# Kernel tuning notes

Measured on AMD Instinct MI355X. Metric: run time of the kernel, lower is better.

The kernel has to match this reference:

```python
import jax, jax.numpy as jnp
import numpy as np

B, S, D = 2, 2048, 1024
H, HD = 16, 64  # num_heads, hidden_size per head


def setup_inputs() -> dict:
    key = jax.random.key(0)
    ks = jax.random.split(key, 10)
    inp = {
        'queries': jax.random.normal(ks[0], (B, S, D), jnp.float32),
        'keys': jax.random.normal(ks[1], (B, S, D), jnp.float32),
        'values': jax.random.normal(ks[2], (B, S, D), jnp.float32),
        # binary indicator masks (some zeros so renorm guard path is exercised)
        'ind_q': (jax.random.uniform(ks[3], (B, S)) > 0.2).astype(jnp.float32),
        'ind_k': (jax.random.uniform(ks[4], (B, S)) > 0.2).astype(jnp.float32),
        'ind_v': (jax.random.uniform(ks[5], (B, S)) > 0.2).astype(jnp.float32),
        'Wq': jax.random.normal(ks[6], (D, H * HD), jnp.float32) / np.sqrt(D),
        'Wk': jax.random.normal(ks[7], (D, H * HD), jnp.float32) / np.sqrt(D),
        'Wv': jax.random.normal(ks[8], (D, H * HD), jnp.float32) / np.sqrt(D),
        'Wo': jax.random.normal(ks[9], (H * HD, D), jnp.float32) / np.sqrt(H * HD),
    }
    return inp


def reference(queries, keys, values, ind_q, ind_k, ind_v, Wq, Wk, Wv, Wo):
    b, nq, _ = queries.shape
    nk = keys.shape[1]
    # projections -> [B, H, S, HD], masked by indicators
    Q = (queries @ Wq).reshape(b, nq, H, HD).transpose(0, 2, 1, 3) * ind_q[:, None, :, None]
    K = (keys @ Wk).reshape(b, nk, H, HD).transpose(0, 2, 1, 3) * ind_k[:, None, :, None]
    V = (values @ Wv).reshape(b, nk, H, HD).transpose(0, 2, 1, 3) * ind_v[:, None, :, None]
    # scaled dot-product scores, plain softmax over keys
    scores = jnp.einsum('bhqd,bhkd->bhqk', Q, K) / jnp.sqrt(jnp.float32(HD))
    attn = jax.nn.softmax(scores, axis=-1)
    # post-softmax multiplicative key-indicator mask + renormalization with zero-row guard
    attn = attn * ind_k[:, None, None, :]
    denom = jnp.sum(attn, axis=-1, keepdims=True)
    attn = attn / jnp.where(denom == 0.0, 1.0, denom)
    out = jnp.einsum('bhqk,bhkd->bhqd', attn, V)  # [B, H, Q, HD]
    out = out.transpose(0, 2, 1, 3).reshape(b, nq, H * HD)
    return out @ Wo
```

## Files before the change

### kernel.cpp

```cpp
#include <hip/hip_runtime.h>
#include <math.h>

typedef __attribute__((ext_vector_type(8))) short bf16x8;
typedef __attribute__((ext_vector_type(4))) float f32x4;

__device__ __forceinline__ unsigned short f2b(float f) {
    union { float f; unsigned int u; } v; v.f = f;
    unsigned int u = v.u + 0x7FFFu + ((v.u >> 16) & 1u);
    return (unsigned short)(u >> 16);
}

__device__ __forceinline__ f32x4 mfma16(bf16x8 a, bf16x8 b, f32x4 c) {
    return __builtin_amdgcn_mfma_f32_16x16x32_bf16(a, b, c, 0, 0, 0);
}

__device__ __forceinline__ void async_ld16(void* l, const void* g) {
    __builtin_amdgcn_global_load_lds(
        (__attribute__((address_space(1))) void*)g,
        (__attribute__((address_space(3))) void*)l, 16, 0, 0);
}

__device__ __forceinline__ float exp2_hw(float x) {
    float r; asm("v_exp_f32 %0, %1" : "=v"(r) : "v"(x)); return r;
}

__device__ __forceinline__ unsigned int cvtpk_bf16(float a, float b) {
    unsigned int r;
    asm("v_cvt_pk_bf16_f32 %0, %1, %2" : "=v"(r) : "v"(a), "v"(b));
    return r;
}

__global__ __launch_bounds__(256) void cvt3(
    const float* __restrict__ q, const float* __restrict__ k,
    const float* __restrict__ v, unsigned short* __restrict__ qo,
    unsigned short* __restrict__ ko, unsigned short* __restrict__ vo)
{
    const int z = blockIdx.z;
    const float* in = (z == 0) ? q : (z == 1) ? k : v;
    unsigned short* out = (z == 0) ? qo : (z == 1) ? ko : vo;
    const int i = (blockIdx.x * 256 + threadIdx.x) * 4;
    const float4 x = *(const float4*)(in + i);
    ushort4 o; o.x = f2b(x.x); o.y = f2b(x.y); o.z = f2b(x.z); o.w = f2b(x.w);
    *(ushort4*)(out + i) = o;
}

__global__ __launch_bounds__(256) void cvt_tr(
    const float* __restrict__ W0, const float* __restrict__ W1,
    const float* __restrict__ W2, const float* __restrict__ W3,
    unsigned short* __restrict__ T0, unsigned short* __restrict__ T1,
    unsigned short* __restrict__ T2, unsigned short* __restrict__ T3)
{
    const int z = blockIdx.z;
    const float* W = (z == 0) ? W0 : (z == 1) ? W1 : (z == 2) ? W2 : W3;
    unsigned short* T = (z == 0) ? T0 : (z == 1) ? T1 : (z == 2) ? T2 : T3;
    __shared__ short Ls[64 * 65];
    const int t = threadIdx.x;
    const int k0 = blockIdx.x * 64, n0 = blockIdx.y * 64;
#pragma unroll
    for (int ii = 0; ii < 4; ++ii) {
        const int kl = (t >> 4) + 16 * ii, nl = (t & 15) * 4;
        const float4 v = *(const float4*)&W[(size_t)(k0 + kl) * 1024 + n0 + nl];
        Ls[kl * 65 + nl + 0] = (short)f2b(v.x);
        Ls[kl * 65 + nl + 1] = (short)f2b(v.y);
        Ls[kl * 65 + nl + 2] = (short)f2b(v.z);
        Ls[kl * 65 + nl + 3] = (short)f2b(v.w);
    }
    __syncthreads();
#pragma unroll
    for (int ii = 0; ii < 4; ++ii) {
        const int nl = (t >> 4) + 16 * ii, kl = (t & 15) * 4;
        ushort4 o;
        o.x = (unsigned short)Ls[(kl + 0) * 65 + nl];
        o.y = (unsigned short)Ls[(kl + 1) * 65 + nl];
        o.z = (unsigned short)Ls[(kl + 2) * 65 + nl];
        o.w = (unsigned short)Ls[(kl + 3) * 65 + nl];
        *(ushort4*)&T[(size_t)(n0 + nl) * 1024 + k0 + kl] = o;
    }
}

__global__ __launch_bounds__(256) void gemm_proj3(
    const unsigned short* __restrict__ qb, const unsigned short* __restrict__ kb,
    const unsigned short* __restrict__ vb,
    const unsigned short* __restrict__ Wqt, const unsigned short* __restrict__ Wkt,
    const unsigned short* __restrict__ Wvt,
    unsigned short* __restrict__ Qw, unsigned short* __restrict__ Kw,
    unsigned short* __restrict__ Vw,
    const float* __restrict__ iq, const float* __restrict__ ik,
    const float* __restrict__ iv)
{
    const int z = blockIdx.z;
    const unsigned short* A  = (z == 0) ? qb  : (z == 1) ? kb  : vb;
    const unsigned short* Bt = (z == 0) ? Wqt : (z == 1) ? Wkt : Wvt;
    unsigned short* Cw       = (z == 0) ? Qw  : (z == 1) ? Kw  : Vw;
    const float* msk         = (z == 0) ? iq  : (z == 1) ? ik  : iv;
    const float scale = (z == 0) ? 0.125f * 1.44269504088896f : 1.0f;

    __shared__ __align__(16) short As[128 * 32];
    __shared__ __align__(16) short Bs[128 * 32];
    __shared__ float maskL[128];
    const int t = threadIdx.x;
    const int w = t >> 6, lane = t & 63, l15 = lane & 15, quad = lane >> 4;
    const int wr = w >> 1, wc = w & 1;
    const int n0 = blockIdx.x * 128, m0 = blockIdx.y * 128;
    if (t < 128) maskL[t] = msk[m0 + t] * scale;

    const int srow = lane >> 2, soff = (lane & 3) * 8;

    f32x4 zero4 = {0.f, 0.f, 0.f, 0.f};
    f32x4 acc[4][4];
#pragma unroll
    for (int i = 0; i < 4; ++i)
#pragma unroll
        for (int j = 0; j < 4; ++j) acc[i][j] = zero4;

    for (int k0 = 0; k0 < 1024; k0 += 32) {
        __syncthreads();
#pragma unroll
        for (int i = 0; i < 2; ++i) {
            const int r = 16 * (2 * w + i);
            async_ld16(As + r * 32, A + (size_t)(m0 + r + srow) * 1024 + k0 + soff);
            async_ld16(Bs + r * 32, Bt + (size_t)(n0 + r + srow) * 1024 + k0 + soff);
        }
        __syncthreads();
        bf16x8 af[4], bfr[4];
#pragma unroll
        for (int i = 0; i < 4; ++i)
            af[i] = *(const bf16x8*)&As[(64 * wr + 16 * i + l15) * 32 + 8 * quad];
#pragma unroll
        for (int j = 0; j < 4; ++j)
            bfr[j] = *(const bf16x8*)&Bs[(64 * wc + 16 * j + l15) * 32 + 8 * quad];
#pragma unroll
        for (int i = 0; i < 4; ++i)
#pragma unroll
            for (int j = 0; j < 4; ++j)
                acc[i][j] = mfma16(af[i], bfr[j], acc[i][j]);
    }

    const int h = 2 * blockIdx.x + wc;
#pragma unroll
    for (int i = 0; i < 4; ++i)
#pragma unroll
        for (int j = 0; j < 4; ++j)
#pragma unroll
            for (int reg = 0; reg < 4; ++reg) {
                const int mloc = 64 * wr + 16 * i + 4 * quad + reg;
                const int m = m0 + mloc;
                const int bb = m >> 11, s = m & 2047;
                const int hd = 16 * j + l15;
                Cw[((size_t)(bb * 16 + h) * 2048 + s) * 64 + hd] =
                    f2b(acc[i][j][reg] * maskL[mloc]);
            }
}

__global__ __launch_bounds__(256) void gemm_out(
    const unsigned short* __restrict__ A, const unsigned short* __restrict__ Bt,
    float* __restrict__ C)
{
    __shared__ __align__(16) short As[128 * 32];
    __shared__ __align__(16) short Bs[64 * 32];
    const int t = threadIdx.x;
    const int w = t >> 6, lane = t & 63, l15 = lane & 15, quad = lane >> 4;
    const int wr = w >> 1, wc = w & 1;
    const int n0 = blockIdx.x * 64, m0 = blockIdx.y * 128;
    const int srow = lane >> 2, soff = (lane & 3) * 8;

    f32x4 zero4 = {0.f, 0.f, 0.f, 0.f};
    f32x4 acc[4][2];
#pragma unroll
    for (int i = 0; i < 4; ++i) { acc[i][0] = zero4; acc[i][1] = zero4; }

    for (int k0 = 0; k0 < 1024; k0 += 32) {
        __syncthreads();
#pragma unroll
        for (int i = 0; i < 2; ++i) {
            const int r = 16 * (2 * w + i);
            async_ld16(As + r * 32, A + (size_t)(m0 + r + srow) * 1024 + k0 + soff);
        }
        async_ld16(Bs + (16 * w) * 32, Bt + (size_t)(n0 + 16 * w + srow) * 1024 + k0 + soff);
        __syncthreads();
        bf16x8 af[4], bfr[2];
#pragma unroll
        for (int i = 0; i < 4; ++i)
            af[i] = *(const bf16x8*)&As[(64 * wr + 16 * i + l15) * 32 + 8 * quad];
#pragma unroll
        for (int j = 0; j < 2; ++j)
            bfr[j] = *(const bf16x8*)&Bs[(32 * wc + 16 * j + l15) * 32 + 8 * quad];
#pragma unroll
        for (int i = 0; i < 4; ++i)
#pragma unroll
            for (int j = 0; j < 2; ++j)
                acc[i][j] = mfma16(af[i], bfr[j], acc[i][j]);
    }
#pragma unroll
    for (int i = 0; i < 4; ++i)
#pragma unroll
        for (int j = 0; j < 2; ++j)
#pragma unroll
            for (int reg = 0; reg < 4; ++reg) {
                const int m = m0 + 64 * wr + 16 * i + 4 * quad + reg;
                const int n = n0 + 32 * wc + 16 * j + l15;
                C[(size_t)m * 1024 + n] = acc[i][j][reg];
            }
}

#define GST 72

__global__ __launch_bounds__(512, 4) void attn_mfma(
    const unsigned short* __restrict__ Qw, const unsigned short* __restrict__ Kw,
    const unsigned short* __restrict__ Vw, const float* __restrict__ indk,
    unsigned short* __restrict__ AO)
{
    __shared__ __align__(16) short Ks[2][64 * GST];
    __shared__ __align__(16) short Vt[2][64 * GST];
    __shared__ float Bl[2048];
    const int t = threadIdx.x;
    const int w = t >> 6, lane = t & 63, l15 = lane & 15, quad = lane >> 4;
    const unsigned wg = (blockIdx.x & 7) * 64 + (blockIdx.x >> 3);
    const int q0 = (wg & 15) * 128;
    const int h = (wg >> 4) & 15, b = wg >> 8;
    const size_t base = (size_t)(b * 16 + h) * (2048 * 64);
    const unsigned short* Qb = Qw + base + (size_t)q0 * 64;
    const unsigned short* Kb = Kw + base;
    const unsigned short* Vb = Vw + base;

    bf16x8 qf[2];
    qf[0] = *(const bf16x8*)&Qb[(16 * w + l15) * 64 + 8 * quad];
    qf[1] = *(const bf16x8*)&Qb[(16 * w + l15) * 64 + 32 + 8 * quad];

    {
        const float4 bi = *(const float4*)&indk[b * 2048 + t * 4];
        float4 bo;
        bo.x = (bi.x - 1.f) * 1e30f; bo.y = (bi.y - 1.f) * 1e30f;
        bo.z = (bi.z - 1.f) * 1e30f; bo.w = (bi.w - 1.f) * 1e30f;
        *(float4*)&Bl[t * 4] = bo;
    }

    const int skr = t >> 3, skc = (t & 7) * 8;
    const int slr = skr ^ (((skr >> 3) & 1) << 2);
    const int dq = t >> 5, kp2 = (t & 31) * 2;

    bf16x8 kreg;
    ushort4 vreg[2];
    kreg = *(const bf16x8*)&Kb[(size_t)skr * 64 + skc];
    vreg[0] = *(const ushort4*)&Vb[(size_t)kp2 * 64 + 4 * dq];
    vreg[1] = *(const ushort4*)&Vb[(size_t)(kp2 + 1) * 64 + 4 * dq];

    const int u_ = l15 >> 2, a_ = l15 & 3;
    const int krA = 8 * u_ + 4 * (u_ & 1) + a_;
    const int krB = 8 * u_ + 4 * (1 - (u_ & 1)) + a_;

    f32x4 zero4 = {0.f, 0.f, 0.f, 0.f};
    f32x4 oacc[4];
    oacc[0] = zero4; oacc[1] = zero4; oacc[2] = zero4; oacc[3] = zero4;
    float l_part = 0.f;

    for (int c = 0; c < 32; ++c) {
        const int cur = c & 1;
        *(bf16x8*)&Ks[cur][slr * GST + skc] = kreg;
        {
            const unsigned int* v0d = (const unsigned int*)&vreg[0];
            const unsigned int* v1d = (const unsigned int*)&vreg[1];
            *(unsigned int*)&Vt[cur][(4 * dq + 0) * GST + kp2] =
                __builtin_amdgcn_perm(v1d[0], v0d[0], 0x05040100u);
            *(unsigned int*)&Vt[cur][(4 * dq + 1) * GST + kp2] =
                __builtin_amdgcn_perm(v1d[0], v0d[0], 0x07060302u);
            *(unsigned int*)&Vt[cur][(4 * dq + 2) * GST + kp2] =
                __builtin_amdgcn_perm(v1d[1], v0d[1], 0x05040100u);
            *(unsigned int*)&Vt[cur][(4 * dq + 3) * GST + kp2] =
                __builtin_amdgcn_perm(v1d[1], v0d[1], 0x07060302u);
        }
        __syncthreads();
        {
            const int kn = (c < 31 ? c + 1 : 31) * 64;
            kreg = *(const bf16x8*)&Kb[(size_t)(kn + skr) * 64 + skc];
            vreg[0] = *(const ushort4*)&Vb[(size_t)(kn + kp2) * 64 + 4 * dq];
            vreg[1] = *(const ushort4*)&Vb[(size_t)(kn + kp2 + 1) * 64 + 4 * dq];
        }
        const short* KsC = Ks[cur];
        const short* VtC = Vt[cur];
        const float* BlC = Bl + c * 64;

        f32x4 sacc[4];
#pragma unroll
        for (int g = 0; g < 4; ++g) {
            const float4 bv = *(const float4*)&BlC[32 * (g >> 1) + 4 * (g & 1) + 8 * quad];
            sacc[g][0] = bv.x; sacc[g][1] = bv.y; sacc[g][2] = bv.z; sacc[g][3] = bv.w;
        }
        __builtin_amdgcn_s_setprio(1);
#pragma unroll
        for (int ks = 0; ks < 2; ++ks)
#pragma unroll
            for (int g = 0; g < 4; ++g) {
                const int row = 32 * (g >> 1) + ((g & 1) ? krB : krA);
                const bf16x8 kf = *(const bf16x8*)&KsC[row * GST + 32 * ks + 8 * quad];
                sacc[g] = mfma16(kf, qf[ks], sacc[g]);
            }
        __builtin_amdgcn_s_setprio(0);

        unsigned int dw[4][2];
#pragma unroll
        for (int g = 0; g < 4; ++g) {
#pragma unroll
            for (int r = 0; r < 4; ++r) sacc[g][r] = exp2_hw(sacc[g][r]);
            dw[g][0] = cvtpk_bf16(sacc[g][0], sacc[g][1]);
            dw[g][1] = cvtpk_bf16(sacc[g][2], sacc[g][3]);
        }

        __builtin_amdgcn_s_setprio(1);
#pragma unroll
        for (int ks = 0; ks < 2; ++ks) {
            union { unsigned int u[4]; bf16x8 b; } pc;
            pc.u[0] = dw[2 * ks][0];     pc.u[1] = dw[2 * ks][1];
            pc.u[2] = dw[2 * ks + 1][0]; pc.u[3] = dw[2 * ks + 1][1];
#pragma unroll
            for (int nj = 0; nj < 4; ++nj) {
                const bf16x8 vbf = *(const bf16x8*)
                    &VtC[(16 * nj + l15) * GST + 32 * ks + 8 * quad];
                oacc[nj] = mfma16(pc.b, vbf, oacc[nj]);
            }
        }
        __builtin_amdgcn_s_setprio(0);

        float rg[4];
#pragma unroll
        for (int g = 0; g < 4; ++g)
            rg[g] = (sacc[g][0] + sacc[g][1]) + (sacc[g][2] + sacc[g][3]);
        l_part += (rg[0] + rg[1]) + (rg[2] + rg[3]);
    }

    float l = l_part;
    l += __shfl_xor(l, 16);
    l += __shfl_xor(l, 32);
    const float inv = (l > 0.f) ? 1.f / l : 0.f;
    float invr[4];
#pragma unroll
    for (int r = 0; r < 4; ++r) invr[r] = __shfl(inv, 4 * quad + r);
#pragma unroll
    for (int nj = 0; nj < 4; ++nj)
#pragma unroll
        for (int r = 0; r < 4; ++r) {
            const int row = q0 + 16 * w + 4 * quad + r;
            AO[(size_t)(b * 2048 + row) * 1024 + h * 64 + 16 * nj + l15] =
                f2b(oacc[nj][r] * invr[r]);
        }
}

extern "C" void kernel_launch(void* const* d_in, const int* in_sizes, int n_in,
                              void* d_out, int out_size, void* d_ws, size_t ws_size,
                              hipStream_t stream) {
    const float* q  = (const float*)d_in[0];
    const float* k  = (const float*)d_in[1];
    const float* v  = (const float*)d_in[2];
    const float* iq = (const float*)d_in[3];
    const float* ik = (const float*)d_in[4];
    const float* iv = (const float*)d_in[5];
    const float* Wq = (const float*)d_in[6];
    const float* Wk = (const float*)d_in[7];
    const float* Wv = (const float*)d_in[8];
    const float* Wo = (const float*)d_in[9];
    float* out = (float*)d_out;
    unsigned short* ws = (unsigned short*)d_ws;

    const size_t M1 = 1048576;
    unsigned short* qb  = ws;
    unsigned short* kb  = ws + 4  * M1;
    unsigned short* vb  = ws + 8  * M1;
    unsigned short* Wqt = ws + 12 * M1;
    unsigned short* Wkt = ws + 13 * M1;
    unsigned short* Wvt = ws + 14 * M1;
    unsigned short* Wot = ws + 15 * M1;
    unsigned short* Qw  = ws + 16 * M1;
    unsigned short* Kw  = ws + 20 * M1;
    unsigned short* Vw  = ws + 24 * M1;
    unsigned short* AO  = ws + 28 * M1;

    cvt3<<<dim3(4096, 1, 3), dim3(256), 0, stream>>>(q, k, v, qb, kb, vb);
    cvt_tr<<<dim3(16, 16, 4), dim3(256), 0, stream>>>(Wq, Wk, Wv, Wo, Wqt, Wkt, Wvt, Wot);
    gemm_proj3<<<dim3(8, 32, 3), dim3(256), 0, stream>>>(
        qb, kb, vb, Wqt, Wkt, Wvt, Qw, Kw, Vw, iq, ik, iv);
    attn_mfma<<<dim3(512, 1, 1), dim3(512), 0, stream>>>(Qw, Kw, Vw, ik, AO);
    gemm_out<<<dim3(16, 32), dim3(256), 0, stream>>>(AO, Wot, out);
}
```

Before: 227.4 us.

## Fuse fp32-to-bf16 input conversion into projection GEMM with register-prefetched double buffering

Drops the separate cvt3 kernel and has the projection GEMM read fp32 activations directly, converting them to bf16 in registers before storing to LDS. The main loop now uses double-buffered LDS, with register prefetch of the next K-slice replacing async global-to-LDS loads, and raises wave priority around the MFMA block. This removes one kernel launch plus the write and re-read of a bf16 copy of q/k/v. In exchange, the GEMM reads twice as many bytes for A, uses more registers and LDS, and does the conversion work redundantly across the 8 column blocks.

```diff
diff --git a/kernel.cpp b/kernel.cpp
--- a/kernel.cpp
+++ b/kernel.cpp
@@ -28,20 +28,6 @@
     unsigned int r;
     asm("v_cvt_pk_bf16_f32 %0, %1, %2" : "=v"(r) : "v"(a), "v"(b));
     return r;
-}
-
-__global__ __launch_bounds__(256) void cvt3(
-    const float* __restrict__ q, const float* __restrict__ k,
-    const float* __restrict__ v, unsigned short* __restrict__ qo,
-    unsigned short* __restrict__ ko, unsigned short* __restrict__ vo)
-{
-    const int z = blockIdx.z;
-    const float* in = (z == 0) ? q : (z == 1) ? k : v;
-    unsigned short* out = (z == 0) ? qo : (z == 1) ? ko : vo;
-    const int i = (blockIdx.x * 256 + threadIdx.x) * 4;
-    const float4 x = *(const float4*)(in + i);
-    ushort4 o; o.x = f2b(x.x); o.y = f2b(x.y); o.z = f2b(x.z); o.w = f2b(x.w);
-    *(ushort4*)(out + i) = o;
 }
 
 __global__ __launch_bounds__(256) void cvt_tr(
@@ -79,8 +65,8 @@
 }
 
 __global__ __launch_bounds__(256) void gemm_proj3(
-    const unsigned short* __restrict__ qb, const unsigned short* __restrict__ kb,
-    const unsigned short* __restrict__ vb,
+    const float* __restrict__ qf, const float* __restrict__ kf,
+    const float* __restrict__ vf,
     const unsigned short* __restrict__ Wqt, const unsigned short* __restrict__ Wkt,
     const unsigned short* __restrict__ Wvt,
     unsigned short* __restrict__ Qw, unsigned short* __restrict__ Kw,
@@ -89,14 +75,14 @@
     const float* __restrict__ iv)
 {
     const int z = blockIdx.z;
-    const unsigned short* A  = (z == 0) ? qb  : (z == 1) ? kb  : vb;
+    const float* A           = (z == 0) ? qf  : (z == 1) ? kf  : vf;
     const unsigned short* Bt = (z == 0) ? Wqt : (z == 1) ? Wkt : Wvt;
     unsigned short* Cw       = (z == 0) ? Qw  : (z == 1) ? Kw  : Vw;
     const float* msk         = (z == 0) ? iq  : (z == 1) ? ik  : iv;
     const float scale = (z == 0) ? 0.125f * 1.44269504088896f : 1.0f;
 
-    __shared__ __align__(16) short As[128 * 32];
-    __shared__ __align__(16) short Bs[128 * 32];
+    __shared__ __align__(16) short As[2][128 * 32];
+    __shared__ __align__(16) short Bs[2][128 * 32];
     __shared__ float maskL[128];
     const int t = threadIdx.x;
     const int w = t >> 6, lane = t & 63, l15 = lane & 15, quad = lane >> 4;
@@ -104,7 +90,18 @@
     const int n0 = blockIdx.x * 128, m0 = blockIdx.y * 128;
     if (t < 128) maskL[t] = msk[m0 + t] * scale;
 
-    const int srow = lane >> 2, soff = (lane & 3) * 8;
+    const int ar = t >> 1, ac = (t & 1) * 16;
+    const float* Arow          = A  + (size_t)(m0 + ar) * 1024 + ac;
+    const unsigned short* Brow = Bt + (size_t)(n0 + ar) * 1024 + ac;
+
+    float4 a4[4];
+    bf16x8 b8[2];
+    a4[0] = *(const float4*)(Arow + 0);
+    a4[1] = *(const float4*)(Arow + 4);
+    a4[2] = *(const float4*)(Arow + 8);
+    a4[3] = *(const float4*)(Arow + 12);
+    b8[0] = *(const bf16x8*)(Brow + 0);
+    b8[1] = *(const bf16x8*)(Brow + 8);
 
     f32x4 zero4 = {0.f, 0.f, 0.f, 0.f};
     f32x4 acc[4][4];
@@ -113,27 +110,43 @@
 #pragma unroll
         for (int j = 0; j < 4; ++j) acc[i][j] = zero4;
 
-    for (int k0 = 0; k0 < 1024; k0 += 32) {
+    for (int step = 0; step < 32; ++step) {
+        const int cur = step & 1;
+        {
+            uint4 lo, hi;
+            lo.x = cvtpk_bf16(a4[0].x, a4[0].y); lo.y = cvtpk_bf16(a4[0].z, a4[0].w);
+            lo.z = cvtpk_bf16(a4[1].x, a4[1].y); lo.w = cvtpk_bf16(a4[1].z, a4[1].w);
+            hi.x = cvtpk_bf16(a4[2].x, a4[2].y); hi.y = cvtpk_bf16(a4[2].z, a4[2].w);
+            hi.z = cvtpk_bf16(a4[3].x, a4[3].y); hi.w = cvtpk_bf16(a4[3].z, a4[3].w);
+            *(uint4*)&As[cur][ar * 32 + ac]     = lo;
+            *(uint4*)&As[cur][ar * 32 + ac + 8] = hi;
+            *(bf16x8*)&Bs[cur][ar * 32 + ac]     = b8[0];
+            *(bf16x8*)&Bs[cur][ar * 32 + ac + 8] = b8[1];
+        }
         __syncthreads();
-#pragma unroll
-        for (int i = 0; i < 2; ++i) {
-            const int r = 16 * (2 * w + i);
-            async_ld16(As + r * 32, A + (size_t)(m0 + r + srow) * 1024 + k0 + soff);
-            async_ld16(Bs + r * 32, Bt + (size_t)(n0 + r + srow) * 1024 + k0 + soff);
-        }
-        __syncthreads();
+        {
+            const int kn = (step < 31 ? step + 1 : 31) * 32;
+            a4[0] = *(const float4*)(Arow + kn + 0);
+            a4[1] = *(const float4*)(Arow + kn + 4);
+            a4[2] = *(const float4*)(Arow + kn + 8);
+            a4[3] = *(const float4*)(Arow + kn + 12);
+            b8[0] = *(const bf16x8*)(Brow + kn + 0);
+            b8[1] = *(const bf16x8*)(Brow + kn + 8);
+        }
         bf16x8 af[4], bfr[4];
 #pragma unroll
         for (int i = 0; i < 4; ++i)
-            af[i] = *(const bf16x8*)&As[(64 * wr + 16 * i + l15) * 32 + 8 * quad];
+            af[i] = *(const bf16x8*)&As[cur][(64 * wr + 16 * i + l15) * 32 + 8 * quad];
 #pragma unroll
         for (int j = 0; j < 4; ++j)
-            bfr[j] = *(const bf16x8*)&Bs[(64 * wc + 16 * j + l15) * 32 + 8 * quad];
+            bfr[j] = *(const bf16x8*)&Bs[cur][(64 * wc + 16 * j + l15) * 32 + 8 * quad];
+        __builtin_amdgcn_s_setprio(1);
 #pragma unroll
         for (int i = 0; i < 4; ++i)
 #pragma unroll
             for (int j = 0; j < 4; ++j)
                 acc[i][j] = mfma16(af[i], bfr[j], acc[i][j]);
+        __builtin_amdgcn_s_setprio(0);
     }
 
     const int h = 2 * blockIdx.x + wc;
@@ -362,9 +375,6 @@
     unsigned short* ws = (unsigned short*)d_ws;
 
     const size_t M1 = 1048576;
-    unsigned short* qb  = ws;
-    unsigned short* kb  = ws + 4  * M1;
-    unsigned short* vb  = ws + 8  * M1;
     unsigned short* Wqt = ws + 12 * M1;
     unsigned short* Wkt = ws + 13 * M1;
     unsigned short* Wvt = ws + 14 * M1;
@@ -374,10 +384,9 @@
     unsigned short* Vw  = ws + 24 * M1;
     unsigned short* AO  = ws + 28 * M1;
 
-    cvt3<<<dim3(4096, 1, 3), dim3(256), 0, stream>>>(q, k, v, qb, kb, vb);
     cvt_tr<<<dim3(16, 16, 4), dim3(256), 0, stream>>>(Wq, Wk, Wv, Wo, Wqt, Wkt, Wvt, Wot);
     gemm_proj3<<<dim3(8, 32, 3), dim3(256), 0, stream>>>(
-        qb, kb, vb, Wqt, Wkt, Wvt, Qw, Kw, Vw, iq, ik, iv);
+        q, k, v, Wqt, Wkt, Wvt, Qw, Kw, Vw, iq, ik, iv);
     attn_mfma<<<dim3(512, 1, 1), dim3(512), 0, stream>>>(Qw, Kw, Vw, ik, AO);
     gemm_out<<<dim3(16, 32), dim3(256), 0, stream>>>(AO, Wot, out);
 }
```

Measured after the change: 240.6 us. +5.8%, slower.
